# Performance work log

Measured on AMD Instinct MI355X. Metric: run time of the kernel, lower is better.

## Reference

```python
import jax, jax.numpy as jnp
import numpy as np

B, N = 1024, 32768


def setup_inputs() -> dict:
    key = jax.random.key(0)
    k1, k2 = jax.random.split(key)
    outputs = jax.random.normal(k1, (B, N), dtype=jnp.float32)
    # reference pulse rates in Hz, inside the pulse band (40/60, 250/60) Hz
    u = jax.random.uniform(k2, (B, 1), dtype=jnp.float32)
    targets = 0.8 + 3.1 * u
    return {"outputs": outputs, "targets": targets, "Fs": 20}


def reference(outputs, targets, Fs):
    n = outputs.shape[-1]
    nf = n // 2 + 1
    f = jnp.linspace(0.0, Fs / 2.0, nf, dtype=jnp.float32)  # (F,)
    min_idx = jnp.argmin(jnp.abs(f - 40.0 / 60.0))
    max_idx = jnp.argmin(jnp.abs(f - 250.0 / 60.0))

    # torch.rfft(..., normalized=True) == orthonormal rFFT; P1 = |X|^2
    X = jnp.fft.rfft(outputs, norm="ortho")  # (B, F) complex
    P1 = X.real ** 2 + X.imag ** 2  # (B, F)

    # per-sample nearest freq bin to the reference rate
    ref_idx = jnp.argmin(jnp.abs(f[None, :] - targets), axis=1)  # (B,)

    idx = jnp.arange(nf)[None, :]  # (1, F)
    r = ref_idx[:, None]  # (B, 1)
    # slices [min_idx : ref_idx-1] and [ref_idx+2 : max_idx]
    mask = ((idx >= min_idx) & (idx < r - 1)) | ((idx >= r + 2) & (idx < max_idx))
    denom = (max_idx - min_idx - 3).astype(jnp.float32)
    other_avg = jnp.sum(P1 * mask, axis=1) / denom  # (B,)

    pulse_amp = jnp.take_along_axis(P1, ref_idx[:, None], axis=1)[:, 0]  # (B,)
    losses = -10.0 * jnp.log10(pulse_amp / other_avg)
    return jnp.mean(losses)
```

## Files before the change

kernel.cpp:

```cpp
#include <hip/hip_runtime.h>
#include <hip/hip_fp16.h>
#include <math.h>

#define BROWS 1024
#define NPTS  32768
#define MPTS  16384
#define NTHR  512
#define MIN_IDX 1092
#define MAX_IDX 6827
#define DENOMF  5732.0f


#define LD 140

typedef _Float16 h8 __attribute__((ext_vector_type(8)));
typedef float    f4 __attribute__((ext_vector_type(4)));

#define MFMA(a, b, c) __builtin_amdgcn_mfma_f32_16x16x32_f16((a), (b), (c), 0, 0, 0)


struct Frag { h8 r, i; };

__device__ inline Frag load_frag(const __half2* __restrict__ base) {
    const float4* p = reinterpret_cast<const float4*>(base);
    union { float4 f; _Float16 h[8]; } a, b;
    a.f = p[0]; b.f = p[1];
    Frag fr;
    fr.r = (h8){a.h[0], a.h[2], a.h[4], a.h[6], b.h[0], b.h[2], b.h[4], b.h[6]};
    fr.i = (h8){a.h[1], a.h[3], a.h[5], a.h[7], b.h[1], b.h[3], b.h[5], b.h[7]};
    return fr;
}

__device__ inline void make_F(int row, int kbase, h8& fr, h8& fi) {
    #pragma unroll
    for (int j = 0; j < 8; ++j) {
        int e = (row * (kbase + j)) & 127;
        float ang = -0.04908738521234052f * (float)e;
        float s, c;
        __sincosf(ang, &s, &c);
        fr[j] = (_Float16)c;
        fi[j] = (_Float16)s;
    }
}

__device__ inline float bin_power2(const __half2* __restrict__ C, int k) {
    float2 a  = __half22float2(C[(k >> 7) * LD + (k & 127)]);
    int p = MPTS - k;
    float2 bz = __half22float2(C[(p >> 7) * LD + (p & 127)]);
    float bx = bz.x, by = -bz.y;
    float ex = 0.5f * (a.x + bx), ey = 0.5f * (a.y + by);
    float dx = a.x - bx,          dy = a.y - by;
    float ox = 0.5f * dy,         oy = -0.5f * dx;
    float ang = (-6.283185307179586f / (float)NPTS) * (float)k;
    float c, sn;
    __sincosf(ang, &sn, &c);
    float Xx = ex + ox * c - oy * sn;
    float Xy = ey + ox * sn + oy * c;
    return (Xx * Xx + Xy * Xy) * (1.0f / (float)NPTS);
}

__global__ __launch_bounds__(NTHR, 4) void snr_row_kernel(
        const float* __restrict__ outs,
        const float* __restrict__ targets,
        float* __restrict__ row_loss) {
    __shared__ __align__(16) __half2 bufA[128 * LD];
    __shared__ float red[NTHR / 64];

    const int b    = blockIdx.x;
    const int tid  = threadIdx.x;
    const int lane = tid & 63;
    const int w    = tid >> 6;
    const int r15  = lane & 15;
    const int g    = lane >> 4;
    const float2* row = reinterpret_cast<const float2*>(outs + (size_t)b * NPTS);

    #pragma unroll
    for (int it = 0; it < MPTS / NTHR; ++it) {
        int m = tid + it * NTHR;
        float2 v = row[m];
        bufA[(m & 127) * LD + (m >> 7)] = __floats2half2_rn(v.x, v.y);
    }

    h8 fr[4], fi[4];
    #pragma unroll
    for (int kc = 0; kc < 4; ++kc)
        make_F(16 * w + r15, 32 * kc + 8 * g, fr[kc], fi[kc]);
    __syncthreads();

    __half2 bm[8][4];
    #pragma unroll
    for (int n0 = 0; n0 < 8; ++n0) {
        f4 accr = {0.f, 0.f, 0.f, 0.f}, acci = {0.f, 0.f, 0.f, 0.f};
        #pragma unroll
        for (int kc = 0; kc < 4; ++kc) {
            Frag z = load_frag(&bufA[(16 * n0 + r15) * LD + 32 * kc + 8 * g]);
            h8 fin = -fi[kc];
            accr = MFMA(fr[kc], z.r, accr);
            accr = MFMA(fin,    z.i, accr);
            acci = MFMA(fr[kc], z.i, acci);
            acci = MFMA(fi[kc], z.r, acci);
        }
        #pragma unroll
        for (int v = 0; v < 4; ++v) {
            int k1 = 16 * w + 4 * g + v;
            int n2 = 16 * n0 + r15;
            int e  = (k1 * n2) & 16383;
            float ang = -3.834951969714103e-4f * (float)e;
            float s, c;
            __sincosf(ang, &s, &c);
            bm[n0][v] = __floats2half2_rn(accr[v] * c - acci[v] * s,
                                          accr[v] * s + acci[v] * c);
        }
    }
    __syncthreads();

    #pragma unroll
    for (int n0 = 0; n0 < 8; ++n0)
        #pragma unroll
        for (int v = 0; v < 4; ++v)
            bufA[(16 * w + 4 * g + v) * LD + 16 * n0 + r15] = bm[n0][v];
    __syncthreads();

    __half2 ct[8][4];
    #pragma unroll
    for (int m0 = 0; m0 < 8; ++m0) {
        f4 accr = {0.f, 0.f, 0.f, 0.f}, acci = {0.f, 0.f, 0.f, 0.f};
        #pragma unroll
        for (int kc = 0; kc < 4; ++kc) {
            Frag a = load_frag(&bufA[(16 * m0 + r15) * LD + 32 * kc + 8 * g]);
            h8 ain = -a.i;
            accr = MFMA(a.r, fr[kc], accr);
            accr = MFMA(ain, fi[kc], accr);
            acci = MFMA(a.r, fi[kc], acci);
            acci = MFMA(a.i, fr[kc], acci);
        }
        #pragma unroll
        for (int v = 0; v < 4; ++v)
            ct[m0][v] = __floats2half2_rn(accr[v], acci[v]);
    }
    __syncthreads();

    #pragma unroll
    for (int m0 = 0; m0 < 8; ++m0)
        #pragma unroll
        for (int v = 0; v < 4; ++v)
            bufA[(16 * w + r15) * LD + 16 * m0 + 4 * g + v] = ct[m0][v];
    __syncthreads();

    float local = 0.0f;
    for (int k = MIN_IDX + tid; k < MAX_IDX; k += NTHR)
        local += bin_power2(bufA, k);

    for (int off = 32; off; off >>= 1) local += __shfl_down(local, off);
    if ((tid & 63) == 0) red[w] = local;
    __syncthreads();

    if (tid == 0) {
        float S = 0.0f;
        #pragma unroll
        for (int q = 0; q < NTHR / 64; ++q) S += red[q];

        float tgt = targets[b];
        double kd = (double)tgt * (16384.0 / 10.0);
        int k0 = (int)kd;
        const float stepf = 10.0f / 16384.0f;
        float f0 = (float)k0 * stepf;
        float f1 = (float)(k0 + 1) * stepf;
        float d0 = fabsf(f0 - tgt);
        float d1 = fabsf(f1 - tgt);
        int rr = (d0 <= d1) ? k0 : (k0 + 1);

        float pm1 = bin_power2(bufA, rr - 1);
        float p0  = bin_power2(bufA, rr);
        float pp1 = bin_power2(bufA, rr + 1);
        float other_avg = (S - pm1 - p0 - pp1) * (1.0f / DENOMF);
        row_loss[b] = -10.0f * log10f(p0 / other_avg);
    }
}

__global__ __launch_bounds__(256) void snr_reduce_kernel(
        const float* __restrict__ row_loss, float* __restrict__ out) {
    __shared__ float red[4];
    float s = 0.0f;
    for (int i = threadIdx.x; i < BROWS; i += 256) s += row_loss[i];
    for (int off = 32; off; off >>= 1) s += __shfl_down(s, off);
    if ((threadIdx.x & 63) == 0) red[threadIdx.x >> 6] = s;
    __syncthreads();
    if (threadIdx.x == 0)
        out[0] = (red[0] + red[1] + red[2] + red[3]) * (1.0f / (float)BROWS);
}

extern "C" void kernel_launch(void* const* d_in, const int* in_sizes, int n_in,
                              void* d_out, int out_size, void* d_ws, size_t ws_size,
                              hipStream_t stream) {
    const float* outs    = (const float*)d_in[0];
    const float* targets = (const float*)d_in[1];
    float* ws  = (float*)d_ws;
    float* out = (float*)d_out;

    snr_row_kernel<<<BROWS, NTHR, 0, stream>>>(outs, targets, ws);
    snr_reduce_kernel<<<1, 256, 0, stream>>>(ws, out);
}
```

Baseline: 60.40 us.

## Split LDS into real/imag planes and replace per-element sincos with rotation recurrences

The shared buffer changes from interleaved half2 to separate real and imaginary half planes. MFMA operands can then be loaded as contiguous h8 vectors instead of being gathered and shuffled from pairs. Most per-element sincos calls, for the DFT matrix, the twiddles and the post-processing twiddles, are replaced by complex-rotation recurrences seeded by a single sincos each. This cuts transcendental and permute work, but recurrences accumulate rounding error and the scalar stores of separate halves may add LDS store instructions and bank conflicts. The last stage's half2 writes into the plane buffer reuse the same storage.

After: 66.34 us. 9.8% more time.

```diff
diff --git a/kernel.cpp b/kernel.cpp
--- a/kernel.cpp
+++ b/kernel.cpp
@@ -11,59 +11,50 @@
 #define DENOMF  5732.0f
 
 
-#define LD 140
+#define LDH 136
+#define PLN (128 * LDH)
 
 typedef _Float16 h8 __attribute__((ext_vector_type(8)));
 typedef float    f4 __attribute__((ext_vector_type(4)));
 
 #define MFMA(a, b, c) __builtin_amdgcn_mfma_f32_16x16x32_f16((a), (b), (c), 0, 0, 0)
 
-
-struct Frag { h8 r, i; };
-
-__device__ inline Frag load_frag(const __half2* __restrict__ base) {
-    const float4* p = reinterpret_cast<const float4*>(base);
-    union { float4 f; _Float16 h[8]; } a, b;
-    a.f = p[0]; b.f = p[1];
-    Frag fr;
-    fr.r = (h8){a.h[0], a.h[2], a.h[4], a.h[6], b.h[0], b.h[2], b.h[4], b.h[6]};
-    fr.i = (h8){a.h[1], a.h[3], a.h[5], a.h[7], b.h[1], b.h[3], b.h[5], b.h[7]};
-    return fr;
-}
-
-__device__ inline void make_F(int row, int kbase, h8& fr, h8& fi) {
-    #pragma unroll
-    for (int j = 0; j < 8; ++j) {
-        int e = (row * (kbase + j)) & 127;
-        float ang = -0.04908738521234052f * (float)e;
-        float s, c;
-        __sincosf(ang, &s, &c);
-        fr[j] = (_Float16)c;
-        fi[j] = (_Float16)s;
-    }
-}
-
-__device__ inline float bin_power2(const __half2* __restrict__ C, int k) {
-    float2 a  = __half22float2(C[(k >> 7) * LD + (k & 127)]);
+#define ANG128 (-0.04908738521234052f)
+#define ANG16K (-3.834951969714103e-4f)
+#define ANG32K (-1.9174759848570515e-4f)
+#define GRC 0.9951847266721969f
+#define GRS (-0.09801714032956060f)
+
+
+__device__ inline h8 ldf(const __half* p) {
+    return *reinterpret_cast<const h8*>(p);
+}
+
+__device__ inline float bin_pow(const __half2* __restrict__ C, int k,
+                                float c, float sn) {
+    float2 a  = __half22float2(C[(k >> 7) * LDH + (k & 127)]);
     int p = MPTS - k;
-    float2 bz = __half22float2(C[(p >> 7) * LD + (p & 127)]);
+    float2 bz = __half22float2(C[(p >> 7) * LDH + (p & 127)]);
     float bx = bz.x, by = -bz.y;
     float ex = 0.5f * (a.x + bx), ey = 0.5f * (a.y + by);
     float dx = a.x - bx,          dy = a.y - by;
     float ox = 0.5f * dy,         oy = -0.5f * dx;
-    float ang = (-6.283185307179586f / (float)NPTS) * (float)k;
-    float c, sn;
-    __sincosf(ang, &sn, &c);
     float Xx = ex + ox * c - oy * sn;
     float Xy = ey + ox * sn + oy * c;
     return (Xx * Xx + Xy * Xy) * (1.0f / (float)NPTS);
+}
+
+__device__ inline float bin_pow_sc(const __half2* __restrict__ C, int k) {
+    float c, sn;
+    __sincosf(ANG32K * (float)k, &sn, &c);
+    return bin_pow(C, k, c, sn);
 }
 
 __global__ __launch_bounds__(NTHR, 4) void snr_row_kernel(
         const float* __restrict__ outs,
         const float* __restrict__ targets,
         float* __restrict__ row_loss) {
-    __shared__ __align__(16) __half2 bufA[128 * LD];
+    __shared__ __align__(16) __half pl[2 * PLN];
     __shared__ float red[NTHR / 64];
 
     const int b    = blockIdx.x;
@@ -78,14 +69,40 @@
     for (int it = 0; it < MPTS / NTHR; ++it) {
         int m = tid + it * NTHR;
         float2 v = row[m];
-        bufA[(m & 127) * LD + (m >> 7)] = __floats2half2_rn(v.x, v.y);
+        int idx = (m & 127) * LDH + (m >> 7);
+        pl[idx]       = (__half)v.x;
+        pl[PLN + idx] = (__half)v.y;
     }
 
     h8 fr[4], fi[4];
-    #pragma unroll
-    for (int kc = 0; kc < 4; ++kc)
-        make_F(16 * w + r15, 32 * kc + 8 * g, fr[kc], fi[kc]);
-    __syncthreads();
+    {
+        const int frow = 16 * w + r15;
+        float stc, sts;
+        __sincosf(ANG128 * (float)frow, &sts, &stc);
+        #pragma unroll
+        for (int kc = 0; kc < 4; ++kc) {
+            int e0 = (frow * (32 * kc + 8 * g)) & 127;
+            float c, s;
+            __sincosf(ANG128 * (float)e0, &s, &c);
+            #pragma unroll
+            for (int j = 0; j < 8; ++j) {
+                fr[kc][j] = (_Float16)c;
+                fi[kc][j] = (_Float16)s;
+                float nc = c * stc - s * sts;
+                s = c * sts + s * stc;
+                c = nc;
+            }
+        }
+    }
+    __syncthreads();
+
+    float tc[4], ts[4], uc[4], us[4];
+    #pragma unroll
+    for (int v = 0; v < 4; ++v) {
+        int k1 = 16 * w + 4 * g + v;
+        __sincosf(ANG16K * (float)(k1 * r15), &ts[v], &tc[v]);
+        __sincosf(ANG16K * (float)(16 * k1), &us[v], &uc[v]);
+    }
 
     __half2 bm[8][4];
     #pragma unroll
@@ -93,23 +110,23 @@
         f4 accr = {0.f, 0.f, 0.f, 0.f}, acci = {0.f, 0.f, 0.f, 0.f};
         #pragma unroll
         for (int kc = 0; kc < 4; ++kc) {
-            Frag z = load_frag(&bufA[(16 * n0 + r15) * LD + 32 * kc + 8 * g]);
+            int base = (16 * n0 + r15) * LDH + 32 * kc + 8 * g;
+            h8 zr = ldf(&pl[base]);
+            h8 zi = ldf(&pl[PLN + base]);
             h8 fin = -fi[kc];
-            accr = MFMA(fr[kc], z.r, accr);
-            accr = MFMA(fin,    z.i, accr);
-            acci = MFMA(fr[kc], z.i, acci);
-            acci = MFMA(fi[kc], z.r, acci);
+            accr = MFMA(fr[kc], zr, accr);
+            accr = MFMA(fin,    zi, accr);
+            acci = MFMA(fr[kc], zi, acci);
+            acci = MFMA(fi[kc], zr, acci);
         }
         #pragma unroll
         for (int v = 0; v < 4; ++v) {
-            int k1 = 16 * w + 4 * g + v;
-            int n2 = 16 * n0 + r15;
-            int e  = (k1 * n2) & 16383;
-            float ang = -3.834951969714103e-4f * (float)e;
-            float s, c;
-            __sincosf(ang, &s, &c);
-            bm[n0][v] = __floats2half2_rn(accr[v] * c - acci[v] * s,
-                                          accr[v] * s + acci[v] * c);
+            float br = accr[v] * tc[v] - acci[v] * ts[v];
+            float bi = accr[v] * ts[v] + acci[v] * tc[v];
+            bm[n0][v] = __floats2half2_rn(br, bi);
+            float nc = tc[v] * uc[v] - ts[v] * us[v];
+            ts[v] = tc[v] * us[v] + ts[v] * uc[v];
+            tc[v] = nc;
         }
     }
     __syncthreads();
@@ -117,8 +134,11 @@
     #pragma unroll
     for (int n0 = 0; n0 < 8; ++n0)
         #pragma unroll
-        for (int v = 0; v < 4; ++v)
-            bufA[(16 * w + 4 * g + v) * LD + 16 * n0 + r15] = bm[n0][v];
+        for (int v = 0; v < 4; ++v) {
+            int idx = (16 * w + 4 * g + v) * LDH + 16 * n0 + r15;
+            pl[idx]       = __low2half(bm[n0][v]);
+            pl[PLN + idx] = __high2half(bm[n0][v]);
+        }
     __syncthreads();
 
     __half2 ct[8][4];
@@ -127,12 +147,14 @@
         f4 accr = {0.f, 0.f, 0.f, 0.f}, acci = {0.f, 0.f, 0.f, 0.f};
         #pragma unroll
         for (int kc = 0; kc < 4; ++kc) {
-            Frag a = load_frag(&bufA[(16 * m0 + r15) * LD + 32 * kc + 8 * g]);
-            h8 ain = -a.i;
-            accr = MFMA(a.r, fr[kc], accr);
+            int base = (16 * m0 + r15) * LDH + 32 * kc + 8 * g;
+            h8 ar = ldf(&pl[base]);
+            h8 ai = ldf(&pl[PLN + base]);
+            h8 ain = -ai;
+            accr = MFMA(ar,  fr[kc], accr);
             accr = MFMA(ain, fi[kc], accr);
-            acci = MFMA(a.r, fi[kc], acci);
-            acci = MFMA(a.i, fr[kc], acci);
+            acci = MFMA(ar,  fi[kc], acci);
+            acci = MFMA(ai,  fr[kc], acci);
         }
         #pragma unroll
         for (int v = 0; v < 4; ++v)
@@ -140,17 +162,26 @@
     }
     __syncthreads();
 
+    __half2* C = reinterpret_cast<__half2*>(pl);
     #pragma unroll
     for (int m0 = 0; m0 < 8; ++m0)
         #pragma unroll
         for (int v = 0; v < 4; ++v)
-            bufA[(16 * w + r15) * LD + 16 * m0 + 4 * g + v] = ct[m0][v];
+            C[(16 * w + r15) * LDH + 16 * m0 + 4 * g + v] = ct[m0][v];
     __syncthreads();
 
     float local = 0.0f;
-    for (int k = MIN_IDX + tid; k < MAX_IDX; k += NTHR)
-        local += bin_power2(bufA, k);
-
+    {
+        int k = MIN_IDX + tid;
+        float cc, ss;
+        __sincosf(ANG32K * (float)k, &ss, &cc);
+        for (; k < MAX_IDX; k += NTHR) {
+            local += bin_pow(C, k, cc, ss);
+            float nc = cc * GRC - ss * GRS;
+            ss = cc * GRS + ss * GRC;
+            cc = nc;
+        }
+    }
     for (int off = 32; off; off >>= 1) local += __shfl_down(local, off);
     if ((tid & 63) == 0) red[w] = local;
     __syncthreads();
@@ -170,9 +201,9 @@
         float d1 = fabsf(f1 - tgt);
         int rr = (d0 <= d1) ? k0 : (k0 + 1);
 
-        float pm1 = bin_power2(bufA, rr - 1);
-        float p0  = bin_power2(bufA, rr);
-        float pp1 = bin_power2(bufA, rr + 1);
+        float pm1 = bin_pow_sc(C, rr - 1);
+        float p0  = bin_pow_sc(C, rr);
+        float pp1 = bin_pow_sc(C, rr + 1);
         float other_avg = (S - pm1 - p0 - pp1) * (1.0f / DENOMF);
         row_loss[b] = -10.0f * log10f(p0 / other_avg);
     }
```
